# Kernel optimization log

Measured on AMD Instinct MI355X. Metric: run time of the kernel, lower is better.

The kernel has to match this reference:

```python
import jax, jax.numpy as jnp
import numpy as np

N_TBINS = 1024
K = 8
B = 32768
IRF_SIGMA = 10.0
PEAK_FACTOR = 5.0
# IRF1DLayer: circular pad (pad_l=N//2, pad_r=N//2-1 for even N) then conv1d with
# flip(irf)  ==  circular convolution with irf followed by roll of -(N-1-N//2).
ROLL_C = N_TBINS - 1 - N_TBINS // 2  # 511


def _wrapped_gaussian(n, mu, sigma):
    # circ_shifted gaussian pulse: wrap tails around the domain, normalize to unit area
    t = np.arange(n, dtype=np.float64)
    g = np.zeros(n, dtype=np.float64)
    for s in (-n, 0, n):
        g += np.exp(-((t - mu + s) ** 2) / (2.0 * sigma ** 2))
    g /= g.sum()
    return jnp.asarray(g, dtype=jnp.float32)


def _circ_conv(x, irf):
    # faithful IRF1DLayer: circular convolution, recentered
    y = jnp.fft.irfft(jnp.fft.rfft(x, axis=-1) * jnp.fft.rfft(irf), n=N_TBINS, axis=-1)
    return jnp.roll(y, -ROLL_C, axis=-1)


def setup_inputs():
    key = jax.random.key(0)
    k1, k2, k3, k4 = jax.random.split(key, 4)
    illumination = _wrapped_gaussian(N_TBINS, N_TBINS // 2, 30.0)  # Gaussian1DLayer buffer
    irf = _wrapped_gaussian(N_TBINS, (N_TBINS - 1) // 2, IRF_SIGMA)
    photon_counts = jax.random.uniform(k1, (B,), jnp.float32, 10.0, 1000.0)
    sbrs = jax.random.uniform(k2, (B,), jnp.float32, 0.1, 1.0)
    bins = jax.random.randint(k3, (B,), 0, N_TBINS)
    cmat_weight = jax.random.normal(k4, (K, N_TBINS), jnp.float32) * 0.05  # Conv1d(k, n_tbins, 1) weight
    return {"illumination": illumination, "photon_counts": photon_counts,
            "sbrs": sbrs, "irf": irf, "cmat_weight": cmat_weight, "bins": bins}


def reference(illumination, photon_counts, sbrs, irf, cmat_weight, bins):
    n = N_TBINS
    inp = _circ_conv(jax.nn.relu(illumination), irf)          # [N] = irf(relu(illum))
    shifts = (bins % n).astype(jnp.int32)                     # [B]
    amb_per_bin = (photon_counts / sbrs) / n                  # [B]
    area = jnp.sum(inp)                                       # current_area
    scale = photon_counts / area                              # [B]
    scaled = inp[None, :] * scale[:, None]                    # [B, N]
    clamped = jnp.minimum(scaled, (PEAK_FACTOR * photon_counts)[:, None])
    offset = clamped + amb_per_bin[:, None]                   # [B, N]
    conv = _circ_conv(offset, irf)                            # [B, N] (batched FFT conv)
    # torch.roll(x, s): out[t] = x[(t - s) % N], vectorized over batch
    idx = (jnp.arange(n)[None, :] - shifts[:, None]) % n      # [B, N]
    shifted = jnp.take_along_axis(conv, idx, axis=1)          # [B, N]
    rate = jax.lax.stop_gradient(shifted)                     # torch.poisson detaches
    noisy = jax.random.poisson(jax.random.key(42), rate, shape=rate.shape).astype(jnp.float32)
    # cmat1D: Conv1d(in=n_tbins, out=k, kernel=1) on [B, N, 1] -> [B, K, 1]
    out = jnp.einsum('bn,kn->bk', noisy, cmat_weight)[..., None]
    return out
```

## Files before the change

kernel.cpp:

```cpp
#include <hip/hip_runtime.h>
#include <hip/hip_bf16.h>
#include <stdint.h>

#define N_T   1024
#define ROLLC 511
#define KCH   8
#define KN_LEV 48
#define RJ_LEV 24
#define CH_N  (2*KN_LEV + 4*RJ_LEV)

__device__ double   g_inp[N_T];
__device__ double   g_conv2[N_T];
__device__ double   g_area;
__device__ uint32_t g_chains[CH_N];
__device__ int      g_T;
__device__ float    g_ll5, g_aa5, g_bb5, g_inva5, g_vr5;

struct TF2 { uint32_t x, y; };

__device__ __forceinline__ TF2 tf2x32(uint32_t k0, uint32_t k1, uint32_t c0, uint32_t c1) {
  uint32_t ks2 = k0 ^ k1 ^ 0x1BD11BDAu;
  uint32_t x0 = c0 + k0, x1 = c1 + k1;
#define TFR(r) { x0 += x1; x1 = (x1 << (r)) | (x1 >> (32 - (r))); x1 ^= x0; }
  TFR(13) TFR(15) TFR(26) TFR(6)
  x0 += k1;  x1 += ks2 + 1u;
  TFR(17) TFR(29) TFR(16) TFR(24)
  x0 += ks2; x1 += k0 + 2u;
  TFR(13) TFR(15) TFR(26) TFR(6)
  x0 += k0;  x1 += k1 + 3u;
  TFR(17) TFR(29) TFR(16) TFR(24)
  x0 += k1;  x1 += ks2 + 4u;
  TFR(13) TFR(15) TFR(26) TFR(6)
  x0 += ks2; x1 += k0 + 5u;
#undef TFR
  return {x0, x1};
}

__device__ __forceinline__ float u01_from_key(uint32_t sk0, uint32_t sk1, uint32_t m) {
  TF2 r = tf2x32(sk0, sk1, 0u, m);
  uint32_t bits = r.x ^ r.y;
  return __uint_as_float((bits >> 9) | 0x3f800000u) - 1.0f;
}

__device__ __forceinline__ float lgamma_xla(float x) {
#pragma clang fp contract(off)
  float z = x - 1.0f;
  float sum = 1.0f;
  sum = sum + 676.5203681218851f     / (z + 1.0f);
  sum = sum + -1259.1392167224028f   / (z + 2.0f);
  sum = sum + 771.32342877765313f    / (z + 3.0f);
  sum = sum + -176.61502916214059f   / (z + 4.0f);
  sum = sum + 12.507343278686905f    / (z + 5.0f);
  sum = sum + -0.13857109526572012f  / (z + 6.0f);
  sum = sum + 9.9843695780195716e-6f / (z + 7.0f);
  sum = sum + 1.5056327351493116e-7f / (z + 8.0f);
  float t = 7.5f + z;
  float log_t = 2.0149030205422647f + log1pf(z / 7.5f);
  return 0.91893853320467274f + (z + 0.5f - t / log_t) * log_t + logf(sum);
}

__device__ __forceinline__ void rej_constants(float lam, float* ll, float* aa, float* bb,
                                              float* inva, float* vr) {
#pragma clang fp contract(off)
  *ll = logf(lam);
  float b = 0.931f + 2.53f * sqrtf(lam);
  float a = -0.059f + 0.02483f * b;
  *bb = b; *aa = a;
  *inva = 1.1239f + 1.1328f / (b - 3.4f);
  *vr = 0.9277f - 3.6224f / (b - 2.0f);
}

__device__ __forceinline__ int ptrs_quick(float lamr, float aa, float bb, float vr,
                                          float u, float v) {
#pragma clang fp contract(off)
  float us = 0.5f - fabsf(u);
  float kf = floorf((2.0f * aa / us + bb) * u + lamr + 0.43f);
  if ((us >= 0.07f) && (v <= vr)) return 1;
  if ((kf < 0.0f) || ((us < 0.013f) && (v > us))) return -1;
  return 0;
}

__device__ __forceinline__ bool ptrs_slow(float lamr, float ll, float aa, float bb,
                                          float inva, float u, float v) {
#pragma clang fp contract(off)
  float us = 0.5f - fabsf(u);
  float kf = floorf((2.0f * aa / us + bb) * u + lamr + 0.43f);
  float s = logf(v * inva / (aa / (us * us) + bb));
  float t = (-lamr + kf * ll) - lgamma_xla(kf + 1.0f);
  return s <= t;
}

__device__ __forceinline__ bool rej_iter(float lam, float ll, float aa, float bb,
                                         float inva, float vr, float u, float v, float* kf) {
#pragma clang fp contract(off)
  float us = 0.5f - fabsf(u);
  float k = floorf((2.0f * aa / us + bb) * u + lam + 0.43f);
  *kf = k;
  if ((us >= 0.07f) && (v <= vr)) return true;
  if ((k < 0.0f) || ((us < 0.013f) && (v > us))) return false;
  float s = logf(v * inva / (aa / (us * us) + bb));
  float t = (-lam + k * ll) - lgamma_xla(k + 1.0f);
  return s <= t;
}

__global__ void __launch_bounds__(128)
pre1_kernel(const float* __restrict__ illum, const float* __restrict__ irf) {
  __shared__ double xs[N_T], irfs[N_T];
  const int tid = threadIdx.x;
  for (int i = tid; i < N_T; i += 128) {
    xs[i]   = fmax((double)illum[i], 0.0);
    irfs[i] = (double)irf[i];
  }
  __syncthreads();
  const int t  = blockIdx.x * 128 + tid;
  const int tt = (t + ROLLC) & (N_T - 1);
  double acc = 0.0;
  for (int j = 0; j < N_T; ++j) acc += xs[j] * irfs[(tt - j) & (N_T - 1)];
  g_inp[t] = acc;
}

__global__ void __launch_bounds__(128)
pre2_kernel(const float* __restrict__ irf, uint32_t* __restrict__ wcount) {
  __shared__ double inps[N_T], irfs[N_T];
  const int tid = threadIdx.x;
  if (blockIdx.x < 8) {
    for (int i = tid; i < N_T; i += 128) {
      inps[i] = g_inp[i];
      irfs[i] = (double)irf[i];
    }
    __syncthreads();
    const int t  = blockIdx.x * 128 + tid;
    const int tt = (t + ROLLC) & (N_T - 1);
    double acc = 0.0;
    for (int j = 0; j < N_T; ++j) acc += inps[j] * irfs[(tt - j) & (N_T - 1)];
    g_conv2[t] = acc;
  } else {
    if (tid == 0) {
      g_T = 1;
      wcount[0] = 0u;
      double area = 0.0;
      for (int j = 0; j < N_T; ++j) area += g_inp[j];
      g_area = area;
    } else if (tid == 1) {
      uint32_t r0 = 0u, r1 = 42u;
      for (int j = 0; j < KN_LEV; ++j) {
        TF2 sub = tf2x32(r0, r1, 0u, 1u);
        TF2 nxt = tf2x32(r0, r1, 0u, 0u);
        g_chains[2*j] = sub.x; g_chains[2*j+1] = sub.y;
        r0 = nxt.x; r1 = nxt.y;
      }
    } else if (tid == 2) {
      uint32_t c0 = 0u, c1 = 42u;
      for (int j = 0; j < RJ_LEV; ++j) {
        TF2 nxt = tf2x32(c0, c1, 0u, 0u);
        TF2 s0  = tf2x32(c0, c1, 0u, 1u);
        TF2 s1  = tf2x32(c0, c1, 0u, 2u);
        int base = 2*KN_LEV + 4*j;
        g_chains[base]   = s0.x; g_chains[base+1] = s0.y;
        g_chains[base+2] = s1.x; g_chains[base+3] = s1.y;
        c0 = nxt.x; c1 = nxt.y;
      }
    } else if (tid == 3) {
      float ll, aa, bb, inva, vr;
      rej_constants(1e5f, &ll, &aa, &bb, &inva, &vr);
      g_ll5 = ll; g_aa5 = aa; g_bb5 = bb; g_inva5 = inva; g_vr5 = vr;
    }
  }
}

__global__ void __launch_bounds__(256)
kA_kernel(const float* __restrict__ photon, const float* __restrict__ sbr,
          const int* __restrict__ bins, const float* __restrict__ w,
          float* __restrict__ out, uint32_t* __restrict__ wcount,
          uint2* __restrict__ recs, uint32_t cap) {
  __shared__ uint32_t ch[CH_N];
  __shared__ uint2    sstage[N_T];
  __shared__ uint16_t tpk[N_T];
  __shared__ float    tlp[N_T];
  __shared__ uint32_t scnts[4];
  __shared__ uint32_t sbase;
  __shared__ float    wred[4][KCH];
  const int b = blockIdx.x, tid = threadIdx.x;
  const int wv = tid >> 6, lane = tid & 63;
  for (int i = tid; i < CH_N; i += 256) ch[i] = g_chains[i];
  __syncthreads();

  const float  ph = photon[b], sb = sbr[b];
  const int    shift = bins[b] & (N_T - 1);
  const double scale = (double)ph / g_area;
  const float  r1f = ph / sb;
  const double amb = (double)r1f * (1.0 / 1024.0);
  const uint32_t mbase = (uint32_t)b << 10;
  const uint32_t ka0 = ch[2*KN_LEV+0], ka1 = ch[2*KN_LEV+1];
  const uint32_t kc0 = ch[2*KN_LEV+2], kc1 = ch[2*KN_LEV+3];
  const float ll5 = g_ll5, aa5 = g_aa5, bb5 = g_bb5, inva5 = g_inva5, vr5 = g_vr5;
  const unsigned long long lmask = (1ull << lane) - 1ull;

  uint32_t wcS = 0;
  uint32_t wcT = 0;
  float acc[KCH];
#pragma unroll
  for (int k = 0; k < KCH; ++k) acc[k] = 0.0f;

  for (int i2 = 0; i2 < 4; ++i2) {
    const int t   = (wv << 8) + (i2 << 6) + lane;
    const int src = (t - shift) & (N_T - 1);
    const float lam = (float)(scale * g_conv2[src] + amb);
    const bool  isRej = (lam >= 10.0f);
    const float lamr  = isRej ? lam : 1e5f;
    const uint32_t m  = mbase + (uint32_t)t;

    float u = u01_from_key(ka0, ka1, m) - 0.5f;
    float v = u01_from_key(kc0, kc1, m);
    float bbq, aaq, vrq;
    {
#pragma clang fp contract(off)
      float b2 = 0.931f + 2.53f * sqrtf(lamr);
      float aq = -0.059f + 0.02483f * b2;
      float vq = 0.9277f - 3.6224f / (b2 - 2.0f);
      bbq = isRej ? b2 : bb5;
      aaq = isRej ? aq : aa5;
      vrq = isRej ? vq : vr5;
    }
    int cls = ptrs_quick(lamr, aaq, bbq, vrq, u, v);
    bool surv;
    if (cls == 0) {
      float ll   = isRej ? logf(lamr) : ll5;
      float inva;
      {
#pragma clang fp contract(off)
        inva = isRej ? (1.1239f + 1.1328f / (bbq - 3.4f)) : inva5;
      }
      surv = !ptrs_slow(lamr, ll, aaq, bbq, inva, u, v);
    } else {
      surv = (cls < 0);
    }
    {
      unsigned long long vote = __ballot(surv);
      uint32_t slot = wcS + (uint32_t)__popcll(vote & lmask);
      if (surv) sstage[(wv << 8) + slot] = make_uint2(m, __float_as_uint(lamr));
      wcS += (uint32_t)__popcll(vote);
    }

    const bool kn = !isRej;
    const float neg = kn ? -lam : 1.0f;
    float glam = kn ? lam : 0.0f;
#pragma unroll
    for (int off = 32; off > 0; off >>= 1) glam = fmaxf(glam, __shfl_xor(glam, off, 64));
    int D = 0;
    if (glam > 0.0f) {
      D = (int)(glam + 2.0f * sqrtf(glam)) + 2;
      if (D > KN_LEV) D = KN_LEV;
    }
    float lp = 0.0f; int k = 0;
    for (int j = 0; j < D; ++j) {
      k += (lp > neg) ? 1 : 0;
      lp += __logf(u01_from_key(ch[2*j], ch[2*j+1], m));
    }
    const bool alive = kn && (lp > neg);
    const float cntf = (kn && !alive) ? (float)(k - 1) : 0.0f;
#pragma unroll
    for (int kk = 0; kk < KCH; ++kk) acc[kk] += cntf * w[kk * N_T + t];
    {
      unsigned long long vote = __ballot(alive);
      uint32_t slot = wcT + (uint32_t)__popcll(vote & lmask);
      if (alive) { tpk[(wv << 8) + slot] = (uint16_t)(((uint32_t)k << 10) | (uint32_t)t);
                   tlp[(wv << 8) + slot] = lp; }
      wcT += (uint32_t)__popcll(vote);
    }
  }

  for (uint32_t i = lane; i < wcT; i += 64) {
    const uint32_t pk = tpk[(wv << 8) + i];
    const uint32_t t  = pk & 1023u;
    int k = (int)(pk >> 10);
    float lp = tlp[(wv << 8) + i];
    const int src = ((int)t - shift) & (N_T - 1);
    const float lam = (float)(scale * g_conv2[src] + amb);
    const float neg = -lam;
    const uint32_t m = mbase + t;
    int j = k;
#pragma unroll 1
    while ((lp > neg) && (j < KN_LEV)) {
      ++k;
      lp += __logf(u01_from_key(ch[2*j], ch[2*j+1], m));
      ++j;
    }
    const float cntf = (float)(k - 1);
#pragma unroll
    for (int kk = 0; kk < KCH; ++kk) acc[kk] += cntf * w[kk * N_T + t];
  }

#pragma unroll
  for (int kk = 0; kk < KCH; ++kk) {
    float vv = acc[kk];
    for (int off = 32; off > 0; off >>= 1) vv += __shfl_down(vv, off, 64);
    if (lane == 0) wred[wv][kk] = vv;
  }
  if (lane == 0) scnts[wv] = wcS;
  __syncthreads();
  if (tid == 0) sbase = atomicAdd(wcount, scnts[0] + scnts[1] + scnts[2] + scnts[3]);
  if (tid < KCH)
    out[b * KCH + tid] = wred[0][tid] + wred[1][tid] + wred[2][tid] + wred[3][tid];
  __syncthreads();
  uint32_t pre = 0;
  for (int ww = 0; ww < wv; ++ww) pre += scnts[ww];
  const uint32_t base = sbase + pre;
  for (uint32_t i = lane; i < wcS; i += 64) {
    const uint32_t g = base + i;
    const uint2 r = sstage[(wv << 8) + i];
    if (g < cap) {
      recs[g] = r;
    } else {
      const uint32_t m = r.x; const float lamr = __uint_as_float(r.y);
      float ll, aaf, bbf, invaf, vrf;
      if (lamr == 1e5f) { ll = ll5; aaf = aa5; bbf = bb5; invaf = inva5; vrf = vr5; }
      else rej_constants(lamr, &ll, &aaf, &bbf, &invaf, &vrf);
      int jf = RJ_LEV;
#pragma unroll 1
      for (int j = 1; j < RJ_LEV; ++j) {
        float uu = u01_from_key(ch[2*KN_LEV + 4*j], ch[2*KN_LEV + 4*j + 1], m) - 0.5f;
        float vv = u01_from_key(ch[2*KN_LEV + 4*j + 2], ch[2*KN_LEV + 4*j + 3], m);
        float kk;
        if (rej_iter(lamr, ll, aaf, bbf, invaf, vrf, uu, vv, &kk)) { jf = j + 1; break; }
      }
      atomicMax(&g_T, jf);
    }
  }
}

__global__ void __launch_bounds__(256)
t2_kernel(const uint32_t* __restrict__ wcount, const uint2* __restrict__ recs, uint32_t cap) {
  __shared__ uint32_t chs[4*RJ_LEV];
  __shared__ int bmax;
  const int tid = threadIdx.x;
  if (tid < 4*RJ_LEV) chs[tid] = g_chains[2*KN_LEV + tid];
  if (tid == 0) bmax = 1;
  __syncthreads();
  uint32_t n = *wcount; if (n > cap) n = cap;
  const float ll5 = g_ll5, aa5 = g_aa5, bb5 = g_bb5, inva5 = g_inva5, vr5 = g_vr5;
  int mymax = 1;
  for (uint32_t gi = blockIdx.x * 256u + tid; gi < n; gi += gridDim.x * 256u) {
    uint2 r = recs[gi];
    const uint32_t m = r.x; const float lamr = __uint_as_float(r.y);
    float ll, aa, bbv, inva, vr;
    if (lamr == 1e5f) { ll = ll5; aa = aa5; bbv = bb5; inva = inva5; vr = vr5; }
    else rej_constants(lamr, &ll, &aa, &bbv, &inva, &vr);
    int jf = RJ_LEV;
#pragma unroll 1
    for (int j = 1; j < RJ_LEV; ++j) {
      float uu = u01_from_key(chs[4*j], chs[4*j+1], m) - 0.5f;
      float vv = u01_from_key(chs[4*j+2], chs[4*j+3], m);
      float kk;
      if (rej_iter(lamr, ll, aa, bbv, inva, vr, uu, vv, &kk)) { jf = j + 1; break; }
    }
    mymax = max(mymax, jf);
  }
  for (int off = 32; off > 0; off >>= 1) mymax = max(mymax, __shfl_down(mymax, off, 64));
  if ((tid & 63) == 0) atomicMax(&bmax, mymax);
  __syncthreads();
  if (tid == 0) atomicMax(&g_T, bmax);
}

__global__ void __launch_bounds__(256)
kB_kernel(const float* __restrict__ photon, const float* __restrict__ sbr,
          const int* __restrict__ bins, const float* __restrict__ w,
          float* __restrict__ out) {
  __shared__ int haveRej;
  __shared__ float wred[4][KCH];
  const int b = blockIdx.x, tid = threadIdx.x;
  const int wv = tid >> 6, lane = tid & 63;
  if (tid == 0) haveRej = 0;
  __syncthreads();
  const float  ph = photon[b], sb = sbr[b];
  const int    shift = bins[b] & (N_T - 1);
  const double scale = (double)ph / g_area;
  const float  r1f = ph / sb;
  const double amb = (double)r1f * (1.0 / 1024.0);
  const uint32_t mbase = (uint32_t)b << 10;
  const int T = g_T;

  float acc[KCH];
#pragma unroll
  for (int k = 0; k < KCH; ++k) acc[k] = 0.0f;
  bool any = false;

  for (int i2 = 0; i2 < 4; ++i2) {
    const int t   = (wv << 8) + (i2 << 6) + lane;
    const int src = (t - shift) & (N_T - 1);
    const float lam = (float)(scale * g_conv2[src] + amb);
    if (lam >= 10.0f) {
      any = true;
      const uint32_t m = mbase + (uint32_t)t;
      float ll, aa, bbv, inva, vr;
      rej_constants(lam, &ll, &aa, &bbv, &inva, &vr);
      float kout = -1.0f;
      bool found = false;
#pragma unroll 1
      for (int jj = T - 1; jj >= 0 && !found; jj -= 4) {
        float kf0, kf1, kf2, kf3;
        bool a0 = false, a1 = false, a2 = false, a3 = false;
        {
          const uint32_t* c = g_chains + 2*KN_LEV + 4*jj;
          a0 = rej_iter(lam, ll, aa, bbv, inva, vr,
                        u01_from_key(c[0], c[1], m) - 0.5f,
                        u01_from_key(c[2], c[3], m), &kf0);
        }
        if (jj - 1 >= 0) {
          const uint32_t* c = g_chains + 2*KN_LEV + 4*(jj-1);
          a1 = rej_iter(lam, ll, aa, bbv, inva, vr,
                        u01_from_key(c[0], c[1], m) - 0.5f,
                        u01_from_key(c[2], c[3], m), &kf1);
        }
        if (jj - 2 >= 0) {
          const uint32_t* c = g_chains + 2*KN_LEV + 4*(jj-2);
          a2 = rej_iter(lam, ll, aa, bbv, inva, vr,
                        u01_from_key(c[0], c[1], m) - 0.5f,
                        u01_from_key(c[2], c[3], m), &kf2);
        }
        if (jj - 3 >= 0) {
          const uint32_t* c = g_chains + 2*KN_LEV + 4*(jj-3);
          a3 = rej_iter(lam, ll, aa, bbv, inva, vr,
                        u01_from_key(c[0], c[1], m) - 0.5f,
                        u01_from_key(c[2], c[3], m), &kf3);
        }
        if      (a0) { kout = kf0; found = true; }
        else if (a1) { kout = kf1; found = true; }
        else if (a2) { kout = kf2; found = true; }
        else if (a3) { kout = kf3; found = true; }
      }
#pragma unroll
      for (int kk = 0; kk < KCH; ++kk) acc[kk] += kout * w[kk * N_T + t];
    }
  }

  if (any) haveRej = 1;
  __syncthreads();
  if (!haveRej) return;
#pragma unroll
  for (int kk = 0; kk < KCH; ++kk) {
    float vv = acc[kk];
    for (int off = 32; off > 0; off >>= 1) vv += __shfl_down(vv, off, 64);
    if (lane == 0) wred[wv][kk] = vv;
  }
  __syncthreads();
  if (tid < KCH)
    atomicAdd(&out[b * KCH + tid], wred[0][tid] + wred[1][tid] + wred[2][tid] + wred[3][tid]);
}

extern "C" void kernel_launch(void* const* d_in, const int* in_sizes, int n_in,
                              void* d_out, int out_size, void* d_ws, size_t ws_size,
                              hipStream_t stream) {
  (void)n_in; (void)out_size;
  const float* illum  = (const float*)d_in[0];
  const float* photon = (const float*)d_in[1];
  const float* sbr    = (const float*)d_in[2];
  const float* irf    = (const float*)d_in[3];
  const float* w      = (const float*)d_in[4];
  const int*   bins   = (const int*)d_in[5];
  float* out = (float*)d_out;
  const int B = in_sizes[1];

  uint32_t* wcount = (uint32_t*)d_ws;
  uint2*    recs   = (uint2*)((char*)d_ws + 16);
  uint32_t  cap    = (ws_size > 16) ? (uint32_t)((ws_size - 16) / sizeof(uint2)) : 0u;

  pre1_kernel<<<8, 128, 0, stream>>>(illum, irf);
  pre2_kernel<<<9, 128, 0, stream>>>(irf, wcount);
  kA_kernel<<<B, 256, 0, stream>>>(photon, sbr, bins, w, out, wcount, recs, cap);
  t2_kernel<<<2048, 256, 0, stream>>>(wcount, recs, cap);
  kB_kernel<<<B, 256, 0, stream>>>(photon, sbr, bins, w, out);
}
```

Baseline: 1.316 ms.

## Compact rejection-sampler elements in kA and process them as a flat list in kB

kA now collects the (index, lambda) pairs that need rejection sampling into a compacted workspace list. kB becomes a flat grid-stride loop over that list, with per-element atomicAdd into the output, instead of rescanning all B×1024 elements per block. If the list would overflow the workspace, kB falls back to a full scan. The Knuth path in kA also generates four Threefry streams interleaved for ILP (u01x4) and hoists the Knuth loop over all four sub-tiles, with launch bounds raised to request higher occupancy. The cost is extra shared-memory staging, more global atomics and some load imbalance in the backward pass.

```diff
diff --git a/kernel.cpp b/kernel.cpp
--- a/kernel.cpp
+++ b/kernel.cpp
@@ -36,6 +36,32 @@
   return {x0, x1};
 }
 
+__device__ __forceinline__ void u01x4(uint32_t k0, uint32_t k1,
+                                      const uint32_t m[4], float u[4]) {
+  const uint32_t ks2 = k0 ^ k1 ^ 0x1BD11BDAu;
+  uint32_t x0[4], x1[4];
+#pragma unroll
+  for (int q = 0; q < 4; ++q) { x0[q] = k0; x1[q] = m[q] + k1; }
+#define RR(r) { _Pragma("unroll") for (int q = 0; q < 4; ++q) { \
+    x0[q] += x1[q]; x1[q] = (x1[q] << (r)) | (x1[q] >> (32 - (r))); x1[q] ^= x0[q]; } }
+#define KI(a_, b_) { _Pragma("unroll") for (int q = 0; q < 4; ++q) { x0[q] += (a_); x1[q] += (b_); } }
+  RR(13) RR(15) RR(26) RR(6)
+  KI(k1, ks2 + 1u)
+  RR(17) RR(29) RR(16) RR(24)
+  KI(ks2, k0 + 2u)
+  RR(13) RR(15) RR(26) RR(6)
+  KI(k0, k1 + 3u)
+  RR(17) RR(29) RR(16) RR(24)
+  KI(k1, ks2 + 4u)
+  RR(13) RR(15) RR(26) RR(6)
+  KI(ks2, k0 + 5u)
+#undef RR
+#undef KI
+#pragma unroll
+  for (int q = 0; q < 4; ++q)
+    u[q] = __uint_as_float((((x0[q] ^ x1[q]) >> 9) | 0x3f800000u)) - 1.0f;
+}
+
 __device__ __forceinline__ float u01_from_key(uint32_t sk0, uint32_t sk1, uint32_t m) {
   TF2 r = tf2x32(sk0, sk1, 0u, m);
   uint32_t bits = r.x ^ r.y;
@@ -103,6 +129,43 @@
   return s <= t;
 }
 
+__device__ __forceinline__ float rej_backward(float lam, uint32_t m, int T) {
+  float ll, aa, bbv, inva, vr;
+  rej_constants(lam, &ll, &aa, &bbv, &inva, &vr);
+  float kout = -1.0f;
+  bool found = false;
+#pragma unroll 1
+  for (int jj = T - 1; jj >= 0 && !found; jj -= 4) {
+    float kf0, kf1, kf2, kf3;
+    bool a0 = false, a1 = false, a2 = false, a3 = false;
+    {
+      const uint32_t* c = g_chains + 2*KN_LEV + 4*jj;
+      a0 = rej_iter(lam, ll, aa, bbv, inva, vr,
+                    u01_from_key(c[0], c[1], m) - 0.5f, u01_from_key(c[2], c[3], m), &kf0);
+    }
+    if (jj - 1 >= 0) {
+      const uint32_t* c = g_chains + 2*KN_LEV + 4*(jj-1);
+      a1 = rej_iter(lam, ll, aa, bbv, inva, vr,
+                    u01_from_key(c[0], c[1], m) - 0.5f, u01_from_key(c[2], c[3], m), &kf1);
+    }
+    if (jj - 2 >= 0) {
+      const uint32_t* c = g_chains + 2*KN_LEV + 4*(jj-2);
+      a2 = rej_iter(lam, ll, aa, bbv, inva, vr,
+                    u01_from_key(c[0], c[1], m) - 0.5f, u01_from_key(c[2], c[3], m), &kf2);
+    }
+    if (jj - 3 >= 0) {
+      const uint32_t* c = g_chains + 2*KN_LEV + 4*(jj-3);
+      a3 = rej_iter(lam, ll, aa, bbv, inva, vr,
+                    u01_from_key(c[0], c[1], m) - 0.5f, u01_from_key(c[2], c[3], m), &kf3);
+    }
+    if      (a0) { kout = kf0; found = true; }
+    else if (a1) { kout = kf1; found = true; }
+    else if (a2) { kout = kf2; found = true; }
+    else if (a3) { kout = kf3; found = true; }
+  }
+  return kout;
+}
+
 __global__ void __launch_bounds__(128)
 pre1_kernel(const float* __restrict__ illum, const float* __restrict__ irf) {
   __shared__ double xs[N_T], irfs[N_T];
@@ -120,7 +183,7 @@
 }
 
 __global__ void __launch_bounds__(128)
-pre2_kernel(const float* __restrict__ irf, uint32_t* __restrict__ wcount) {
+pre2_kernel(const float* __restrict__ irf, uint32_t* __restrict__ hdr) {
   __shared__ double inps[N_T], irfs[N_T];
   const int tid = threadIdx.x;
   if (blockIdx.x < 8) {
@@ -137,7 +200,7 @@
   } else {
     if (tid == 0) {
       g_T = 1;
-      wcount[0] = 0u;
+      hdr[0] = 0u; hdr[1] = 0u; hdr[2] = 0u;
       double area = 0.0;
       for (int j = 0; j < N_T; ++j) area += g_inp[j];
       g_area = area;
@@ -168,17 +231,18 @@
   }
 }
 
-__global__ void __launch_bounds__(256)
+__global__ void __launch_bounds__(256, 4)
 kA_kernel(const float* __restrict__ photon, const float* __restrict__ sbr,
           const int* __restrict__ bins, const float* __restrict__ w,
-          float* __restrict__ out, uint32_t* __restrict__ wcount,
-          uint2* __restrict__ recs, uint32_t cap) {
+          float* __restrict__ out, uint32_t* __restrict__ hdr,
+          uint2* __restrict__ recs, uint32_t capS, uint32_t rmax) {
   __shared__ uint32_t ch[CH_N];
   __shared__ uint2    sstage[N_T];
+  __shared__ uint2    rstage[N_T];
   __shared__ uint16_t tpk[N_T];
   __shared__ float    tlp[N_T];
-  __shared__ uint32_t scnts[4];
-  __shared__ uint32_t sbase;
+  __shared__ uint32_t scnts[4], rcnts[4];
+  __shared__ uint32_t sbase, rbase;
   __shared__ float    wred[4][KCH];
   const int b = blockIdx.x, tid = threadIdx.x;
   const int wv = tid >> 6, lane = tid & 63;
@@ -196,40 +260,46 @@
   const float ll5 = g_ll5, aa5 = g_aa5, bb5 = g_bb5, inva5 = g_inva5, vr5 = g_vr5;
   const unsigned long long lmask = (1ull << lane) - 1ull;
 
-  uint32_t wcS = 0;
-  uint32_t wcT = 0;
-  float acc[KCH];
-#pragma unroll
-  for (int k = 0; k < KCH; ++k) acc[k] = 0.0f;
-
-  for (int i2 = 0; i2 < 4; ++i2) {
-    const int t   = (wv << 8) + (i2 << 6) + lane;
+  uint32_t m4[4]; float lam4[4]; float neg4[4]; bool isR[4];
+  float glam = 0.0f;
+#pragma unroll
+  for (int q = 0; q < 4; ++q) {
+    const int t   = (wv << 8) + (q << 6) + lane;
     const int src = (t - shift) & (N_T - 1);
     const float lam = (float)(scale * g_conv2[src] + amb);
-    const bool  isRej = (lam >= 10.0f);
-    const float lamr  = isRej ? lam : 1e5f;
-    const uint32_t m  = mbase + (uint32_t)t;
-
-    float u = u01_from_key(ka0, ka1, m) - 0.5f;
-    float v = u01_from_key(kc0, kc1, m);
+    lam4[q] = lam; m4[q] = mbase + (uint32_t)t;
+    isR[q]  = (lam >= 10.0f);
+    neg4[q] = isR[q] ? 1.0f : -lam;
+    glam = fmaxf(glam, isR[q] ? 0.0f : lam);
+  }
+
+  float u4[4], v4[4];
+  u01x4(ka0, ka1, m4, u4);
+  u01x4(kc0, kc1, m4, v4);
+
+  uint32_t wcS = 0, wcR = 0, wcT = 0;
+#pragma unroll
+  for (int q = 0; q < 4; ++q) {
+    const float lamr = isR[q] ? lam4[q] : 1e5f;
+    const float u = u4[q] - 0.5f, v = v4[q];
     float bbq, aaq, vrq;
     {
 #pragma clang fp contract(off)
       float b2 = 0.931f + 2.53f * sqrtf(lamr);
       float aq = -0.059f + 0.02483f * b2;
       float vq = 0.9277f - 3.6224f / (b2 - 2.0f);
-      bbq = isRej ? b2 : bb5;
-      aaq = isRej ? aq : aa5;
-      vrq = isRej ? vq : vr5;
+      bbq = isR[q] ? b2 : bb5;
+      aaq = isR[q] ? aq : aa5;
+      vrq = isR[q] ? vq : vr5;
     }
     int cls = ptrs_quick(lamr, aaq, bbq, vrq, u, v);
     bool surv;
     if (cls == 0) {
-      float ll   = isRej ? logf(lamr) : ll5;
+      float ll = isR[q] ? logf(lamr) : ll5;
       float inva;
       {
 #pragma clang fp contract(off)
-        inva = isRej ? (1.1239f + 1.1328f / (bbq - 3.4f)) : inva5;
+        inva = isR[q] ? (1.1239f + 1.1328f / (bbq - 3.4f)) : inva5;
       }
       surv = !ptrs_slow(lamr, ll, aaq, bbq, inva, u, v);
     } else {
@@ -238,36 +308,53 @@
     {
       unsigned long long vote = __ballot(surv);
       uint32_t slot = wcS + (uint32_t)__popcll(vote & lmask);
-      if (surv) sstage[(wv << 8) + slot] = make_uint2(m, __float_as_uint(lamr));
+      if (surv) sstage[(wv << 8) + slot] = make_uint2(m4[q], __float_as_uint(lamr));
       wcS += (uint32_t)__popcll(vote);
     }
-
-    const bool kn = !isRej;
-    const float neg = kn ? -lam : 1.0f;
-    float glam = kn ? lam : 0.0f;
-#pragma unroll
-    for (int off = 32; off > 0; off >>= 1) glam = fmaxf(glam, __shfl_xor(glam, off, 64));
-    int D = 0;
-    if (glam > 0.0f) {
-      D = (int)(glam + 2.0f * sqrtf(glam)) + 2;
-      if (D > KN_LEV) D = KN_LEV;
-    }
-    float lp = 0.0f; int k = 0;
-    for (int j = 0; j < D; ++j) {
-      k += (lp > neg) ? 1 : 0;
-      lp += __logf(u01_from_key(ch[2*j], ch[2*j+1], m));
-    }
-    const bool alive = kn && (lp > neg);
-    const float cntf = (kn && !alive) ? (float)(k - 1) : 0.0f;
+    {
+      unsigned long long vote = __ballot(isR[q]);
+      uint32_t slot = wcR + (uint32_t)__popcll(vote & lmask);
+      if (isR[q]) rstage[(wv << 8) + slot] = make_uint2(m4[q], __float_as_uint(lam4[q]));
+      wcR += (uint32_t)__popcll(vote);
+    }
+  }
+
+#pragma unroll
+  for (int off = 32; off > 0; off >>= 1) glam = fmaxf(glam, __shfl_xor(glam, off, 64));
+  int D = 0;
+  if (glam > 0.0f) {
+    D = (int)(glam + 2.0f * sqrtf(glam)) + 2;
+    if (D > KN_LEV) D = KN_LEV;
+  }
+  float lp4[4] = {0.0f, 0.0f, 0.0f, 0.0f};
+  int   k4[4]  = {0, 0, 0, 0};
+#pragma unroll 1
+  for (int j = 0; j < D; ++j) {
+    const uint32_t kk0 = ch[2*j], kk1 = ch[2*j+1];
+    u01x4(kk0, kk1, m4, u4);
+#pragma unroll
+    for (int q = 0; q < 4; ++q) {
+      k4[q] += (lp4[q] > neg4[q]) ? 1 : 0;
+      lp4[q] += __logf(u4[q]);
+    }
+  }
+
+  float acc[KCH];
+#pragma unroll
+  for (int k = 0; k < KCH; ++k) acc[k] = 0.0f;
+#pragma unroll
+  for (int q = 0; q < 4; ++q) {
+    const bool kn = !isR[q];
+    const bool alive = kn && (lp4[q] > neg4[q]);
+    const float cntf = (kn && !alive) ? (float)(k4[q] - 1) : 0.0f;
+    const int t = (wv << 8) + (q << 6) + lane;
 #pragma unroll
     for (int kk = 0; kk < KCH; ++kk) acc[kk] += cntf * w[kk * N_T + t];
-    {
-      unsigned long long vote = __ballot(alive);
-      uint32_t slot = wcT + (uint32_t)__popcll(vote & lmask);
-      if (alive) { tpk[(wv << 8) + slot] = (uint16_t)(((uint32_t)k << 10) | (uint32_t)t);
-                   tlp[(wv << 8) + slot] = lp; }
-      wcT += (uint32_t)__popcll(vote);
-    }
+    unsigned long long vote = __ballot(alive);
+    uint32_t slot = wcT + (uint32_t)__popcll(vote & lmask);
+    if (alive) { tpk[(wv << 8) + slot] = (uint16_t)(((uint32_t)k4[q] << 10) | (uint32_t)t);
+                 tlp[(wv << 8) + slot] = lp4[q]; }
+    wcT += (uint32_t)__popcll(vote);
   }
 
   for (uint32_t i = lane; i < wcT; i += 64) {
@@ -297,19 +384,20 @@
     for (int off = 32; off > 0; off >>= 1) vv += __shfl_down(vv, off, 64);
     if (lane == 0) wred[wv][kk] = vv;
   }
-  if (lane == 0) scnts[wv] = wcS;
+  if (lane == 0) { scnts[wv] = wcS; rcnts[wv] = wcR; }
   __syncthreads();
-  if (tid == 0) sbase = atomicAdd(wcount, scnts[0] + scnts[1] + scnts[2] + scnts[3]);
+  if (tid == 0) sbase = atomicAdd(&hdr[0], scnts[0] + scnts[1] + scnts[2] + scnts[3]);
+  if (tid == 1) rbase = atomicAdd(&hdr[1], rcnts[0] + rcnts[1] + rcnts[2] + rcnts[3]);
   if (tid < KCH)
     out[b * KCH + tid] = wred[0][tid] + wred[1][tid] + wred[2][tid] + wred[3][tid];
   __syncthreads();
-  uint32_t pre = 0;
-  for (int ww = 0; ww < wv; ++ww) pre += scnts[ww];
-  const uint32_t base = sbase + pre;
+  uint32_t preS = 0, preR = 0;
+  for (int ww = 0; ww < wv; ++ww) { preS += scnts[ww]; preR += rcnts[ww]; }
+  const uint32_t baseS = sbase + preS;
   for (uint32_t i = lane; i < wcS; i += 64) {
-    const uint32_t g = base + i;
+    const uint32_t g = baseS + i;
     const uint2 r = sstage[(wv << 8) + i];
-    if (g < cap) {
+    if (g < capS) {
       recs[g] = r;
     } else {
       const uint32_t m = r.x; const float lamr = __uint_as_float(r.y);
@@ -327,17 +415,23 @@
       atomicMax(&g_T, jf);
     }
   }
+  const uint32_t baseR = rbase + preR;
+  for (uint32_t i = lane; i < wcR; i += 64) {
+    const uint32_t g = baseR + i;
+    if (g < rmax) recs[capS + g] = rstage[(wv << 8) + i];
+    else hdr[2] = 1u;
+  }
 }
 
 __global__ void __launch_bounds__(256)
-t2_kernel(const uint32_t* __restrict__ wcount, const uint2* __restrict__ recs, uint32_t cap) {
+t2_kernel(const uint32_t* __restrict__ hdr, const uint2* __restrict__ recs, uint32_t capS) {
   __shared__ uint32_t chs[4*RJ_LEV];
   __shared__ int bmax;
   const int tid = threadIdx.x;
   if (tid < 4*RJ_LEV) chs[tid] = g_chains[2*KN_LEV + tid];
   if (tid == 0) bmax = 1;
   __syncthreads();
-  uint32_t n = *wcount; if (n > cap) n = cap;
+  uint32_t n = hdr[0]; if (n > capS) n = capS;
   const float ll5 = g_ll5, aa5 = g_aa5, bb5 = g_bb5, inva5 = g_inva5, vr5 = g_vr5;
   int mymax = 1;
   for (uint32_t gi = blockIdx.x * 256u + tid; gi < n; gi += gridDim.x * 256u) {
@@ -365,87 +459,41 @@
 __global__ void __launch_bounds__(256)
 kB_kernel(const float* __restrict__ photon, const float* __restrict__ sbr,
           const int* __restrict__ bins, const float* __restrict__ w,
-          float* __restrict__ out) {
-  __shared__ int haveRej;
-  __shared__ float wred[4][KCH];
-  const int b = blockIdx.x, tid = threadIdx.x;
-  const int wv = tid >> 6, lane = tid & 63;
-  if (tid == 0) haveRej = 0;
-  __syncthreads();
-  const float  ph = photon[b], sb = sbr[b];
-  const int    shift = bins[b] & (N_T - 1);
-  const double scale = (double)ph / g_area;
-  const float  r1f = ph / sb;
-  const double amb = (double)r1f * (1.0 / 1024.0);
-  const uint32_t mbase = (uint32_t)b << 10;
+          float* __restrict__ out, const uint32_t* __restrict__ hdr,
+          const uint2* __restrict__ recs, uint32_t capS, uint32_t rmax, int B) {
+  const int tid = threadIdx.x;
   const int T = g_T;
-
-  float acc[KCH];
-#pragma unroll
-  for (int k = 0; k < KCH; ++k) acc[k] = 0.0f;
-  bool any = false;
-
-  for (int i2 = 0; i2 < 4; ++i2) {
-    const int t   = (wv << 8) + (i2 << 6) + lane;
-    const int src = (t - shift) & (N_T - 1);
-    const float lam = (float)(scale * g_conv2[src] + amb);
-    if (lam >= 10.0f) {
-      any = true;
-      const uint32_t m = mbase + (uint32_t)t;
-      float ll, aa, bbv, inva, vr;
-      rej_constants(lam, &ll, &aa, &bbv, &inva, &vr);
-      float kout = -1.0f;
-      bool found = false;
-#pragma unroll 1
-      for (int jj = T - 1; jj >= 0 && !found; jj -= 4) {
-        float kf0, kf1, kf2, kf3;
-        bool a0 = false, a1 = false, a2 = false, a3 = false;
-        {
-          const uint32_t* c = g_chains + 2*KN_LEV + 4*jj;
-          a0 = rej_iter(lam, ll, aa, bbv, inva, vr,
-                        u01_from_key(c[0], c[1], m) - 0.5f,
-                        u01_from_key(c[2], c[3], m), &kf0);
-        }
-        if (jj - 1 >= 0) {
-          const uint32_t* c = g_chains + 2*KN_LEV + 4*(jj-1);
-          a1 = rej_iter(lam, ll, aa, bbv, inva, vr,
-                        u01_from_key(c[0], c[1], m) - 0.5f,
-                        u01_from_key(c[2], c[3], m), &kf1);
-        }
-        if (jj - 2 >= 0) {
-          const uint32_t* c = g_chains + 2*KN_LEV + 4*(jj-2);
-          a2 = rej_iter(lam, ll, aa, bbv, inva, vr,
-                        u01_from_key(c[0], c[1], m) - 0.5f,
-                        u01_from_key(c[2], c[3], m), &kf2);
-        }
-        if (jj - 3 >= 0) {
-          const uint32_t* c = g_chains + 2*KN_LEV + 4*(jj-3);
-          a3 = rej_iter(lam, ll, aa, bbv, inva, vr,
-                        u01_from_key(c[0], c[1], m) - 0.5f,
-                        u01_from_key(c[2], c[3], m), &kf3);
-        }
-        if      (a0) { kout = kf0; found = true; }
-        else if (a1) { kout = kf1; found = true; }
-        else if (a2) { kout = kf2; found = true; }
-        else if (a3) { kout = kf3; found = true; }
+  if (hdr[2] == 0u) {
+    uint32_t n = hdr[1]; if (n > rmax) n = rmax;
+    for (uint32_t gi = blockIdx.x * 256u + tid; gi < n; gi += gridDim.x * 256u) {
+      const uint2 r = recs[capS + gi];
+      const uint32_t m = r.x; const float lam = __uint_as_float(r.y);
+      const float kout = rej_backward(lam, m, T);
+      const uint32_t bb_ = m >> 10, tt_ = m & 1023u;
+#pragma unroll
+      for (int kk = 0; kk < KCH; ++kk)
+        atomicAdd(&out[bb_ * KCH + kk], kout * w[kk * N_T + tt_]);
+    }
+  } else {
+    const uint32_t total = (uint32_t)B << 10;
+    for (uint32_t gi = blockIdx.x * 256u + tid; gi < total; gi += gridDim.x * 256u) {
+      const uint32_t bb_ = gi >> 10, tt_ = gi & 1023u;
+      const float ph = photon[bb_], sbv = sbr[bb_];
+      const int shift = bins[bb_] & (N_T - 1);
+      const double scale = (double)ph / g_area;
+      const float r1f = ph / sbv;
+      const double amb = (double)r1f * (1.0 / 1024.0);
+      const int src = ((int)tt_ - shift) & (N_T - 1);
+      const float lam = (float)(scale * g_conv2[src] + amb);
+      if (lam >= 10.0f) {
+        const uint32_t m = (bb_ << 10) + tt_;
+        const float kout = rej_backward(lam, m, T);
+#pragma unroll
+        for (int kk = 0; kk < KCH; ++kk)
+          atomicAdd(&out[bb_ * KCH + kk], kout * w[kk * N_T + tt_]);
       }
-#pragma unroll
-      for (int kk = 0; kk < KCH; ++kk) acc[kk] += kout * w[kk * N_T + t];
-    }
-  }
-
-  if (any) haveRej = 1;
-  __syncthreads();
-  if (!haveRej) return;
-#pragma unroll
-  for (int kk = 0; kk < KCH; ++kk) {
-    float vv = acc[kk];
-    for (int off = 32; off > 0; off >>= 1) vv += __shfl_down(vv, off, 64);
-    if (lane == 0) wred[wv][kk] = vv;
-  }
-  __syncthreads();
-  if (tid < KCH)
-    atomicAdd(&out[b * KCH + tid], wred[0][tid] + wred[1][tid] + wred[2][tid] + wred[3][tid]);
+    }
+  }
 }
 
 extern "C" void kernel_launch(void* const* d_in, const int* in_sizes, int n_in,
@@ -461,13 +509,15 @@
   float* out = (float*)d_out;
   const int B = in_sizes[1];
 
-  uint32_t* wcount = (uint32_t*)d_ws;
-  uint2*    recs   = (uint2*)((char*)d_ws + 16);
-  uint32_t  cap    = (ws_size > 16) ? (uint32_t)((ws_size - 16) / sizeof(uint2)) : 0u;
+  uint32_t* hdr = (uint32_t*)d_ws;
+  uint2*    recs = (uint2*)((char*)d_ws + 16);
+  uint32_t  capTot = (ws_size > 16) ? (uint32_t)((ws_size - 16) / sizeof(uint2)) : 0u;
+  uint32_t  rmax = capTot / 4; if (rmax > 4194304u) rmax = 4194304u;
+  uint32_t  capS = capTot - rmax;
 
   pre1_kernel<<<8, 128, 0, stream>>>(illum, irf);
-  pre2_kernel<<<9, 128, 0, stream>>>(irf, wcount);
-  kA_kernel<<<B, 256, 0, stream>>>(photon, sbr, bins, w, out, wcount, recs, cap);
-  t2_kernel<<<2048, 256, 0, stream>>>(wcount, recs, cap);
-  kB_kernel<<<B, 256, 0, stream>>>(photon, sbr, bins, w, out);
-}
+  pre2_kernel<<<9, 128, 0, stream>>>(irf, hdr);
+  kA_kernel<<<B, 256, 0, stream>>>(photon, sbr, bins, w, out, hdr, recs, capS, rmax);
+  t2_kernel<<<2048, 256, 0, stream>>>(hdr, recs, capS);
+  kB_kernel<<<1024, 256, 0, stream>>>(photon, sbr, bins, w, out, hdr, recs, capS, rmax, B);
+}
```

Result: slower. 1.545 ms (+17.4%).
